# Performance work log

Hardware: AMD Instinct MI355X
Metric: run time of the kernel (lower is better)

The kernel has to match this reference:

```python
import jax, jax.numpy as jnp
import numpy as np

EPS = 1e-5

def layer_norm(x, g, b):
    m = x.mean(-1, keepdims=True)
    v = ((x - m) ** 2).mean(-1, keepdims=True)
    return (x - m) * jax.lax.rsqrt(v + EPS) * g + b

def setup_inputs() -> dict:
    key = jax.random.key(0)
    ks = jax.random.split(key, 12)
    H = 2048; E = 2048; I = 2048; N = 32
    A = (H + E) // 2  # attention hidden = 2048
    s = lambda fan: 1.0 / np.sqrt(fan)
    inp = {
        "input":   jax.random.normal(ks[0], (I,), jnp.float32),
        "hiddens": jax.random.normal(ks[1], (N, H), jnp.float32),
        "cells":   jax.random.normal(ks[2], (N, H), jnp.float32),
        "external":jax.random.normal(ks[3], (E,), jnp.float32),
        # weights (torch nn.Linear layout: [out, in]); LN enabled -> no biases on linears
        "W_ai":   jax.random.uniform(ks[4], (A, H + E), jnp.float32, -s(H+E), s(H+E)),
        "W_attn": jax.random.uniform(ks[5], (1, A), jnp.float32, -s(A), s(A)),
        "W_merge":jax.random.uniform(ks[6], (H, H), jnp.float32, -s(H), s(H)),
        "W_iou":  jax.random.uniform(ks[7], (3 * H, I + H), jnp.float32, -s(I+H), s(I+H)),
        "W_fi":   jax.random.uniform(ks[8], (H, I), jnp.float32, -s(I), s(I)),
        "W_fh":   jax.random.uniform(ks[9], (H, H), jnp.float32, -s(H), s(H)),
        "g_merge": jnp.ones((H,), jnp.float32), "b_merge": jnp.zeros((H,), jnp.float32),
        "g_f": jnp.ones((H,), jnp.float32), "b_f": jnp.zeros((H,), jnp.float32),
        "g_i": jnp.ones((H,), jnp.float32), "b_i": jnp.zeros((H,), jnp.float32),
        "g_o": jnp.ones((H,), jnp.float32), "b_o": jnp.zeros((H,), jnp.float32),
        "g_u": jnp.ones((H,), jnp.float32), "b_u": jnp.zeros((H,), jnp.float32),
        "g_c": jnp.ones((H,), jnp.float32), "b_c": jnp.zeros((H,), jnp.float32),
    }
    return inp

def reference(input, hiddens, cells, external,
              W_ai, W_attn, W_merge, W_iou, W_fi, W_fh,
              g_merge, b_merge, g_f, b_f, g_i, b_i, g_o, b_o, g_u, b_u, g_c, b_c):
    N, H = hiddens.shape
    # forget-gate preactivations: [H] + [N,H] -> [N,H]
    f_lin = input @ W_fi.T + hiddens @ W_fh.T
    # attentive merge over children
    ext = jnp.broadcast_to(external, (N, external.shape[0]))
    ai = jnp.tanh(jnp.concatenate([hiddens, ext], axis=1) @ W_ai.T)       # [N, (H+E)//2]
    attn = jax.nn.softmax(ai @ W_attn.T, axis=0)                          # [N, 1]
    merged = (hiddens * attn).sum(0)                                      # [H]
    merge_hidden = jnp.tanh(layer_norm(merged @ W_merge.T, g_merge, b_merge))
    # i/o/u gates from [input ; merged_hidden]
    iou = jnp.concatenate([input, merge_hidden]) @ W_iou.T                # [3H]
    i_l, o_l, u_l = jnp.split(iou, 3)
    f = jax.nn.sigmoid(layer_norm(f_lin, g_f, b_f))                       # [N,H]
    i = jax.nn.sigmoid(layer_norm(i_l, g_i, b_i))
    o = jax.nn.sigmoid(layer_norm(o_l, g_o, b_o))
    u = jnp.tanh(layer_norm(u_l, g_u, b_u))                               # dropout=0 -> identity
    new_cell = layer_norm(i * u + (f * cells).sum(0), g_c, b_c)           # [H]
    new_h = o * jnp.tanh(new_cell)
    return new_h, new_cell
```

## Files before the change

kernel.cpp:

```cpp
#include <hip/hip_runtime.h>
#include <hip/hip_bf16.h>

typedef __bf16 bf16_t;
typedef __attribute__((ext_vector_type(8))) __bf16 bf16x8;
typedef __attribute__((ext_vector_type(4))) float f32x4;

#define EPSF 1e-5f

__global__ __launch_bounds__(256) void s1_mega(
    const float* __restrict__ hiddens, const float* __restrict__ external,
    const float* __restrict__ input,
    const float* __restrict__ W_ai, const float* __restrict__ W_fh,
    const float* __restrict__ W_fi, const float* __restrict__ W_attn,
    float* __restrict__ lp, float* __restrict__ fh_out, float* __restrict__ fi_out)
{
    __shared__ float red[4][16][16];
    __shared__ float ejs[4][16];

    int b    = blockIdx.x;
    int tid  = threadIdx.x;
    int wave = tid >> 6;
    int lane = tid & 63;

    if (b < 512) {
        bool is_ai = (b < 256);
        int  bb    = is_ai ? b : b - 256;
        int  jt    = bb & 127;
        int  nt    = bb >> 7;
        int  l15   = lane & 15;
        int  quad  = lane >> 4;
        int  k0    = wave * 512;
        int  wstride = is_ai ? 4096 : 2048;
        const float* W = is_ai ? W_ai : W_fh;

        const float* ap = hiddens + (size_t)(nt * 16 + l15) * 2048 + quad * 8 + k0;
        const float* bp = W + (size_t)(jt * 16 + l15) * wstride + quad * 8 + k0;

        f32x4 acc = {0.f, 0.f, 0.f, 0.f};
        float ejacc = 0.f;

        if (is_ai) {
            const float* ep = bp + 2048;
            const float* xp = external + quad * 8 + k0;
            #pragma unroll 2
            for (int k = 0; k < 512; k += 32) {
                float4 a0 = *(const float4*)(ap + k);
                float4 a1 = *(const float4*)(ap + k + 4);
                float4 b0 = *(const float4*)(bp + k);
                float4 b1 = *(const float4*)(bp + k + 4);
                bf16x8 av, bv;
                av[0]=(bf16_t)a0.x; av[1]=(bf16_t)a0.y; av[2]=(bf16_t)a0.z; av[3]=(bf16_t)a0.w;
                av[4]=(bf16_t)a1.x; av[5]=(bf16_t)a1.y; av[6]=(bf16_t)a1.z; av[7]=(bf16_t)a1.w;
                bv[0]=(bf16_t)b0.x; bv[1]=(bf16_t)b0.y; bv[2]=(bf16_t)b0.z; bv[3]=(bf16_t)b0.w;
                bv[4]=(bf16_t)b1.x; bv[5]=(bf16_t)b1.y; bv[6]=(bf16_t)b1.z; bv[7]=(bf16_t)b1.w;
                acc = __builtin_amdgcn_mfma_f32_16x16x32_bf16(av, bv, acc, 0, 0, 0);
                float4 e0 = *(const float4*)(ep + k);
                float4 e1 = *(const float4*)(ep + k + 4);
                float4 x0 = *(const float4*)(xp + k);
                float4 x1 = *(const float4*)(xp + k + 4);
                ejacc += e0.x*x0.x + e0.y*x0.y + e0.z*x0.z + e0.w*x0.w
                       + e1.x*x1.x + e1.y*x1.y + e1.z*x1.z + e1.w*x1.w;
            }
            ejacc += __shfl_xor(ejacc, 16, 64);
            ejacc += __shfl_xor(ejacc, 32, 64);
            if (quad == 0) ejs[wave][l15] = ejacc;
        } else {
            #pragma unroll 4
            for (int k = 0; k < 512; k += 32) {
                float4 a0 = *(const float4*)(ap + k);
                float4 a1 = *(const float4*)(ap + k + 4);
                float4 b0 = *(const float4*)(bp + k);
                float4 b1 = *(const float4*)(bp + k + 4);
                bf16x8 av, bv;
                av[0]=(bf16_t)a0.x; av[1]=(bf16_t)a0.y; av[2]=(bf16_t)a0.z; av[3]=(bf16_t)a0.w;
                av[4]=(bf16_t)a1.x; av[5]=(bf16_t)a1.y; av[6]=(bf16_t)a1.z; av[7]=(bf16_t)a1.w;
                bv[0]=(bf16_t)b0.x; bv[1]=(bf16_t)b0.y; bv[2]=(bf16_t)b0.z; bv[3]=(bf16_t)b0.w;
                bv[4]=(bf16_t)b1.x; bv[5]=(bf16_t)b1.y; bv[6]=(bf16_t)b1.z; bv[7]=(bf16_t)b1.w;
                acc = __builtin_amdgcn_mfma_f32_16x16x32_bf16(av, bv, acc, 0, 0, 0);
            }
        }

        #pragma unroll
        for (int r = 0; r < 4; ++r) red[wave][quad * 4 + r][l15] = acc[r];
        __syncthreads();

        int row = tid >> 4, col = tid & 15;
        float s = red[0][row][col] + red[1][row][col] + red[2][row][col] + red[3][row][col];

        if (is_ai) {
            float ej = ejs[0][col] + ejs[1][col] + ejs[2][col] + ejs[3][col];
            float lg = tanhf(s + ej) * W_attn[jt * 16 + col];
            lg += __shfl_xor(lg, 1, 64);
            lg += __shfl_xor(lg, 2, 64);
            lg += __shfl_xor(lg, 4, 64);
            lg += __shfl_xor(lg, 8, 64);
            if (col == 0) lp[jt * 32 + nt * 16 + row] = lg;
        } else {
            fh_out[(size_t)(nt * 16 + row) * 2048 + jt * 16 + col] = s;
        }
    } else {
        int b2 = b - 512;
        #pragma unroll
        for (int r = 0; r < 4; ++r) {
            int row = b2 * 16 + wave * 4 + r;
            const float4* wp = (const float4*)(W_fi + (size_t)row * 2048) + lane;
            const float4* xp = (const float4*)input + lane;
            float acc2 = 0.f;
            #pragma unroll
            for (int k = 0; k < 512; k += 64) {
                float4 w = wp[k];
                float4 v = xp[k];
                acc2 += w.x*v.x + w.y*v.y + w.z*v.z + w.w*v.w;
            }
            #pragma unroll
            for (int off = 32; off; off >>= 1) acc2 += __shfl_down(acc2, off, 64);
            if (lane == 0) fi_out[row] = acc2;
        }
    }
}

__global__ __launch_bounds__(256) void s2_mega(
    const float* __restrict__ fi, const float* __restrict__ fh,
    const float* __restrict__ lp, const float* __restrict__ hiddens,
    float* __restrict__ frs, float* __restrict__ merged)
{
    __shared__ float s1[256], s2[256];
    int b = blockIdx.x, t = threadIdx.x;

    if (b < 32) {
        int n = b;
        float sum = 0.f, sq = 0.f;
        #pragma unroll
        for (int i = 0; i < 8; ++i) {
            int h = t * 8 + i;
            float v = fi[h] + fh[n * 2048 + h];
            sum += v; sq += v * v;
        }
        s1[t] = sum; s2[t] = sq;
        __syncthreads();
        for (int off = 128; off; off >>= 1) {
            if (t < off) { s1[t] += s1[t + off]; s2[t] += s2[t + off]; }
            __syncthreads();
        }
        if (t == 0) {
            const float inv = 1.f / 2048.f;
            float mean = s1[0] * inv;
            frs[n * 2]     = mean;
            frs[n * 2 + 1] = rsqrtf(s2[0] * inv - mean * mean + EPSF);
        }
    } else {
        __shared__ float lred[32][8];
        __shared__ float attnw[32];
        int n = t >> 3, sl = t & 7;
        float p = 0.f;
        #pragma unroll
        for (int m = 0; m < 16; ++m) p += lp[(sl * 16 + m) * 32 + n];
        lred[n][sl] = p;
        __syncthreads();
        if (sl == 0) {
            float lg = 0.f;
            #pragma unroll
            for (int m = 0; m < 8; ++m) lg += lred[n][m];
            lred[n][0] = lg;
        }
        __syncthreads();
        if (t < 32) {
            float mx = -1e30f;
            for (int m = 0; m < 32; ++m) mx = fmaxf(mx, lred[m][0]);
            float ssum = 0.f;
            for (int m = 0; m < 32; ++m) ssum += expf(lred[m][0] - mx);
            attnw[t] = expf(lred[t][0] - mx) / ssum;
        }
        __syncthreads();
        int h = (b - 32) * 256 + t;
        float acc = 0.f;
        #pragma unroll 8
        for (int n2 = 0; n2 < 32; ++n2) acc += attnw[n2] * hiddens[n2 * 2048 + h];
        merged[h] = acc;
    }
}

__global__ __launch_bounds__(256) void s3_mega(
    const float* __restrict__ W_merge, const float* __restrict__ merged,
    const float* __restrict__ fi, const float* __restrict__ fh,
    const float* __restrict__ frs, const float* __restrict__ gf,
    const float* __restrict__ bf_, const float* __restrict__ cells,
    float* __restrict__ mm, float* __restrict__ fc)
{
    int b = blockIdx.x, t = threadIdx.x;
    if (b < 512) {
        int row  = b * 4 + (t >> 6);
        int lane = t & 63;
        const float4* wp = (const float4*)(W_merge + (size_t)row * 2048) + lane;
        const float4* xp = (const float4*)merged + lane;
        float acc = 0.f;
        #pragma unroll
        for (int k = 0; k < 512; k += 64) {
            float4 w = wp[k];
            float4 v = xp[k];
            acc += w.x*v.x + w.y*v.y + w.z*v.z + w.w*v.w;
        }
        #pragma unroll
        for (int off = 32; off; off >>= 1) acc += __shfl_down(acc, off, 64);
        if (lane == 0) mm[row] = acc;
    } else {
        int h = (b - 512) * 256 + t;
        float g = gf[h], bb = bf_[h], f_i = fi[h];
        float acc = 0.f;
        for (int n = 0; n < 32; ++n) {
            float v = (f_i + fh[n * 2048 + h] - frs[n * 2]) * frs[n * 2 + 1] * g + bb;
            float f = 1.f / (1.f + expf(-v));
            acc += f * cells[n * 2048 + h];
        }
        fc[h] = acc;
    }
}

__global__ __launch_bounds__(256) void s4_iou(
    const float* __restrict__ W_iou, const float* __restrict__ mm,
    const float* __restrict__ input, const float* __restrict__ g,
    const float* __restrict__ bvec, float* __restrict__ iou)
{
    __shared__ float xcat[4096];
    __shared__ float s1[256], s2[256];
    int b = blockIdx.x, t = threadIdx.x;

    float v[8]; float sum = 0.f, sq = 0.f;
    #pragma unroll
    for (int i = 0; i < 8; ++i) {
        v[i] = mm[t * 8 + i]; sum += v[i]; sq += v[i] * v[i];
    }
    s1[t] = sum; s2[t] = sq;
    __syncthreads();
    for (int off = 128; off; off >>= 1) {
        if (t < off) { s1[t] += s1[t + off]; s2[t] += s2[t + off]; }
        __syncthreads();
    }
    const float inv = 1.f / 2048.f;
    float mean = s1[0] * inv;
    float r = rsqrtf(s2[0] * inv - mean * mean + EPSF);
    #pragma unroll
    for (int i = 0; i < 8; ++i) {
        int h = t * 8 + i;
        xcat[h]        = input[h];
        xcat[2048 + h] = tanhf((v[i] - mean) * r * g[h] + bvec[h]);
    }
    __syncthreads();

    int wave = t >> 6, lane = t & 63;
    int row = b * 4 + wave;
    const float4* wp = (const float4*)(W_iou + (size_t)row * 4096) + lane;
    const float4* xp = (const float4*)xcat + lane;
    float acc = 0.f;
    #pragma unroll
    for (int k = 0; k < 1024; k += 64) {
        float4 w = wp[k];
        float4 x = xp[k];
        acc += w.x*x.x + w.y*x.y + w.z*x.z + w.w*x.w;
    }
    #pragma unroll
    for (int off = 32; off; off >>= 1) acc += __shfl_down(acc, off, 64);
    if (lane == 0) iou[row] = acc;
}

__global__ __launch_bounds__(256) void s5_tail(
    const float* __restrict__ iou, const float* __restrict__ fc,
    const float* __restrict__ gi, const float* __restrict__ bi,
    const float* __restrict__ go, const float* __restrict__ bo,
    const float* __restrict__ gu, const float* __restrict__ bu,
    const float* __restrict__ gc, const float* __restrict__ bc,
    float* __restrict__ out)
{
    __shared__ float sA[6][256];
    int t = threadIdx.x;
    float vi[8], vo[8], vu[8];
    float si = 0, qi = 0, so = 0, qo = 0, su = 0, qu = 0;
    #pragma unroll
    for (int i = 0; i < 8; ++i) {
        int h = t * 8 + i;
        vi[i] = iou[h]; vo[i] = iou[2048 + h]; vu[i] = iou[4096 + h];
        si += vi[i]; qi += vi[i] * vi[i];
        so += vo[i]; qo += vo[i] * vo[i];
        su += vu[i]; qu += vu[i] * vu[i];
    }
    sA[0][t] = si; sA[1][t] = qi; sA[2][t] = so;
    sA[3][t] = qo; sA[4][t] = su; sA[5][t] = qu;
    __syncthreads();
    for (int off = 128; off; off >>= 1) {
        if (t < off) {
            #pragma unroll
            for (int c = 0; c < 6; ++c) sA[c][t] += sA[c][t + off];
        }
        __syncthreads();
    }
    const float inv = 1.f / 2048.f;
    float mi = sA[0][0] * inv, ri = rsqrtf(sA[1][0] * inv - mi * mi + EPSF);
    float mo = sA[2][0] * inv, ro = rsqrtf(sA[3][0] * inv - mo * mo + EPSF);
    float mu = sA[4][0] * inv, ru = rsqrtf(sA[5][0] * inv - mu * mu + EPSF);
    __syncthreads();

    float o_[8], v_[8];
    float sv = 0, qv = 0;
    #pragma unroll
    for (int i = 0; i < 8; ++i) {
        int h = t * 8 + i;
        float ivl = 1.f / (1.f + expf(-((vi[i] - mi) * ri * gi[h] + bi[h])));
        o_[i]     = 1.f / (1.f + expf(-((vo[i] - mo) * ro * go[h] + bo[h])));
        float uvl = tanhf((vu[i] - mu) * ru * gu[h] + bu[h]);
        v_[i] = ivl * uvl + fc[h];
        sv += v_[i]; qv += v_[i] * v_[i];
    }
    sA[0][t] = sv; sA[1][t] = qv;
    __syncthreads();
    for (int off = 128; off; off >>= 1) {
        if (t < off) { sA[0][t] += sA[0][t + off]; sA[1][t] += sA[1][t + off]; }
        __syncthreads();
    }
    float mc = sA[0][0] * inv, rc = rsqrtf(sA[1][0] * inv - mc * mc + EPSF);
    #pragma unroll
    for (int i = 0; i < 8; ++i) {
        int h = t * 8 + i;
        float nc = (v_[i] - mc) * rc * gc[h] + bc[h];
        float nh = o_[i] * tanhf(nc);
        out[h]        = nh;
        out[2048 + h] = nc;
    }
}

extern "C" void kernel_launch(void* const* d_in, const int* in_sizes, int n_in,
                              void* d_out, int out_size, void* d_ws, size_t ws_size,
                              hipStream_t stream)
{
    const float* input    = (const float*)d_in[0];
    const float* hiddens  = (const float*)d_in[1];
    const float* cells    = (const float*)d_in[2];
    const float* external = (const float*)d_in[3];
    const float* W_ai     = (const float*)d_in[4];
    const float* W_attn   = (const float*)d_in[5];
    const float* W_merge  = (const float*)d_in[6];
    const float* W_iou    = (const float*)d_in[7];
    const float* W_fi     = (const float*)d_in[8];
    const float* W_fh     = (const float*)d_in[9];
    const float* g_merge  = (const float*)d_in[10];
    const float* b_merge  = (const float*)d_in[11];
    const float* g_f      = (const float*)d_in[12];
    const float* b_f      = (const float*)d_in[13];
    const float* g_i      = (const float*)d_in[14];
    const float* b_i      = (const float*)d_in[15];
    const float* g_o      = (const float*)d_in[16];
    const float* b_o      = (const float*)d_in[17];
    const float* g_u      = (const float*)d_in[18];
    const float* b_u      = (const float*)d_in[19];
    const float* g_c      = (const float*)d_in[20];
    const float* b_c      = (const float*)d_in[21];

    float* ws = (float*)d_ws;
    float* ws_fh     = ws;
    float* ws_fi     = ws + 65536;
    float* ws_lp     = ws + 67584;
    float* ws_frs    = ws + 71680;
    float* ws_merged = ws + 71744;
    float* ws_mm     = ws + 73792;
    float* ws_fc     = ws + 75840;
    float* ws_iou    = ws + 77888;
    float* out = (float*)d_out;

    s1_mega<<<640, 256, 0, stream>>>(hiddens, external, input,
                                     W_ai, W_fh, W_fi, W_attn,
                                     ws_lp, ws_fh, ws_fi);
    s2_mega<<<40, 256, 0, stream>>>(ws_fi, ws_fh, ws_lp, hiddens,
                                    ws_frs, ws_merged);
    s3_mega<<<520, 256, 0, stream>>>(W_merge, ws_merged, ws_fi, ws_fh,
                                     ws_frs, g_f, b_f, cells, ws_mm, ws_fc);
    s4_iou<<<1536, 256, 0, stream>>>(W_iou, ws_mm, input, g_merge, b_merge, ws_iou);
    s5_tail<<<1, 256, 0, stream>>>(ws_iou, ws_fc, g_i, b_i, g_o, b_o,
                                   g_u, b_u, g_c, b_c, out);
}
```

Before: 292.0 us.

## Process both child tiles per block in s1 and two rows per wave in s4

In s1, each MFMA block now computes both 16-row halves of the 32 children against one weight tile, so each W_ai/W_fh tile is loaded once instead of twice. The W_fi GEMV blocks are rebalanced to fill the freed grid slots. In s4, the LayerNorm reduction moves to per-wave shuffles with the activation vector kept in registers instead of shared memory, and each wave handles two rows, halving the grid. This trades higher register pressure and fewer blocks for fewer redundant weight reads and per-block setup passes.

```diff
diff --git a/kernel.cpp b/kernel.cpp
--- a/kernel.cpp
+++ b/kernel.cpp
@@ -14,7 +14,7 @@
     const float* __restrict__ W_fi, const float* __restrict__ W_attn,
     float* __restrict__ lp, float* __restrict__ fh_out, float* __restrict__ fi_out)
 {
-    __shared__ float red[4][16][16];
+    __shared__ float red[4][2][16][16];
     __shared__ float ejs[4][16];
 
     int b    = blockIdx.x;
@@ -22,21 +22,21 @@
     int wave = tid >> 6;
     int lane = tid & 63;
 
-    if (b < 512) {
-        bool is_ai = (b < 256);
-        int  bb    = is_ai ? b : b - 256;
-        int  jt    = bb & 127;
-        int  nt    = bb >> 7;
+    if (b < 256) {
+        bool is_ai = (b < 128);
+        int  jt    = is_ai ? b : b - 128;
         int  l15   = lane & 15;
         int  quad  = lane >> 4;
         int  k0    = wave * 512;
         int  wstride = is_ai ? 4096 : 2048;
         const float* W = is_ai ? W_ai : W_fh;
 
-        const float* ap = hiddens + (size_t)(nt * 16 + l15) * 2048 + quad * 8 + k0;
-        const float* bp = W + (size_t)(jt * 16 + l15) * wstride + quad * 8 + k0;
-
-        f32x4 acc = {0.f, 0.f, 0.f, 0.f};
+        const float* a0p = hiddens + (size_t)l15 * 2048 + quad * 8 + k0;
+        const float* a1p = hiddens + (size_t)(16 + l15) * 2048 + quad * 8 + k0;
+        const float* bp  = W + (size_t)(jt * 16 + l15) * wstride + quad * 8 + k0;
+
+        f32x4 acc0 = {0.f, 0.f, 0.f, 0.f};
+        f32x4 acc1 = {0.f, 0.f, 0.f, 0.f};
         float ejacc = 0.f;
 
         if (is_ai) {
@@ -44,20 +44,25 @@
             const float* xp = external + quad * 8 + k0;
             #pragma unroll 2
             for (int k = 0; k < 512; k += 32) {
-                float4 a0 = *(const float4*)(ap + k);
-                float4 a1 = *(const float4*)(ap + k + 4);
+                float4 p0 = *(const float4*)(a0p + k);
+                float4 p1 = *(const float4*)(a0p + k + 4);
+                float4 q0 = *(const float4*)(a1p + k);
+                float4 q1 = *(const float4*)(a1p + k + 4);
                 float4 b0 = *(const float4*)(bp + k);
                 float4 b1 = *(const float4*)(bp + k + 4);
-                bf16x8 av, bv;
-                av[0]=(bf16_t)a0.x; av[1]=(bf16_t)a0.y; av[2]=(bf16_t)a0.z; av[3]=(bf16_t)a0.w;
-                av[4]=(bf16_t)a1.x; av[5]=(bf16_t)a1.y; av[6]=(bf16_t)a1.z; av[7]=(bf16_t)a1.w;
-                bv[0]=(bf16_t)b0.x; bv[1]=(bf16_t)b0.y; bv[2]=(bf16_t)b0.z; bv[3]=(bf16_t)b0.w;
-                bv[4]=(bf16_t)b1.x; bv[5]=(bf16_t)b1.y; bv[6]=(bf16_t)b1.z; bv[7]=(bf16_t)b1.w;
-                acc = __builtin_amdgcn_mfma_f32_16x16x32_bf16(av, bv, acc, 0, 0, 0);
                 float4 e0 = *(const float4*)(ep + k);
                 float4 e1 = *(const float4*)(ep + k + 4);
                 float4 x0 = *(const float4*)(xp + k);
                 float4 x1 = *(const float4*)(xp + k + 4);
+                bf16x8 av0, av1, bv;
+                av0[0]=(bf16_t)p0.x; av0[1]=(bf16_t)p0.y; av0[2]=(bf16_t)p0.z; av0[3]=(bf16_t)p0.w;
+                av0[4]=(bf16_t)p1.x; av0[5]=(bf16_t)p1.y; av0[6]=(bf16_t)p1.z; av0[7]=(bf16_t)p1.w;
+                av1[0]=(bf16_t)q0.x; av1[1]=(bf16_t)q0.y; av1[2]=(bf16_t)q0.z; av1[3]=(bf16_t)q0.w;
+                av1[4]=(bf16_t)q1.x; av1[5]=(bf16_t)q1.y; av1[6]=(bf16_t)q1.z; av1[7]=(bf16_t)q1.w;
+                bv[0]=(bf16_t)b0.x; bv[1]=(bf16_t)b0.y; bv[2]=(bf16_t)b0.z; bv[3]=(bf16_t)b0.w;
+                bv[4]=(bf16_t)b1.x; bv[5]=(bf16_t)b1.y; bv[6]=(bf16_t)b1.z; bv[7]=(bf16_t)b1.w;
+                acc0 = __builtin_amdgcn_mfma_f32_16x16x32_bf16(av0, bv, acc0, 0, 0, 0);
+                acc1 = __builtin_amdgcn_mfma_f32_16x16x32_bf16(av1, bv, acc1, 0, 0, 0);
                 ejacc += e0.x*x0.x + e0.y*x0.y + e0.z*x0.z + e0.w*x0.w
                        + e1.x*x1.x + e1.y*x1.y + e1.z*x1.z + e1.w*x1.w;
             }
@@ -65,44 +70,57 @@
             ejacc += __shfl_xor(ejacc, 32, 64);
             if (quad == 0) ejs[wave][l15] = ejacc;
         } else {
-            #pragma unroll 4
+            #pragma unroll 2
             for (int k = 0; k < 512; k += 32) {
-                float4 a0 = *(const float4*)(ap + k);
-                float4 a1 = *(const float4*)(ap + k + 4);
+                float4 p0 = *(const float4*)(a0p + k);
+                float4 p1 = *(const float4*)(a0p + k + 4);
+                float4 q0 = *(const float4*)(a1p + k);
+                float4 q1 = *(const float4*)(a1p + k + 4);
                 float4 b0 = *(const float4*)(bp + k);
                 float4 b1 = *(const float4*)(bp + k + 4);
-                bf16x8 av, bv;
-                av[0]=(bf16_t)a0.x; av[1]=(bf16_t)a0.y; av[2]=(bf16_t)a0.z; av[3]=(bf16_t)a0.w;
-                av[4]=(bf16_t)a1.x; av[5]=(bf16_t)a1.y; av[6]=(bf16_t)a1.z; av[7]=(bf16_t)a1.w;
+                bf16x8 av0, av1, bv;
+                av0[0]=(bf16_t)p0.x; av0[1]=(bf16_t)p0.y; av0[2]=(bf16_t)p0.z; av0[3]=(bf16_t)p0.w;
+                av0[4]=(bf16_t)p1.x; av0[5]=(bf16_t)p1.y; av0[6]=(bf16_t)p1.z; av0[7]=(bf16_t)p1.w;
+                av1[0]=(bf16_t)q0.x; av1[1]=(bf16_t)q0.y; av1[2]=(bf16_t)q0.z; av1[3]=(bf16_t)q0.w;
+                av1[4]=(bf16_t)q1.x; av1[5]=(bf16_t)q1.y; av1[6]=(bf16_t)q1.z; av1[7]=(bf16_t)q1.w;
                 bv[0]=(bf16_t)b0.x; bv[1]=(bf16_t)b0.y; bv[2]=(bf16_t)b0.z; bv[3]=(bf16_t)b0.w;
                 bv[4]=(bf16_t)b1.x; bv[5]=(bf16_t)b1.y; bv[6]=(bf16_t)b1.z; bv[7]=(bf16_t)b1.w;
-                acc = __builtin_amdgcn_mfma_f32_16x16x32_bf16(av, bv, acc, 0, 0, 0);
+                acc0 = __builtin_amdgcn_mfma_f32_16x16x32_bf16(av0, bv, acc0, 0, 0, 0);
+                acc1 = __builtin_amdgcn_mfma_f32_16x16x32_bf16(av1, bv, acc1, 0, 0, 0);
             }
         }
 
         #pragma unroll
-        for (int r = 0; r < 4; ++r) red[wave][quad * 4 + r][l15] = acc[r];
+        for (int r = 0; r < 4; ++r) {
+            red[wave][0][quad * 4 + r][l15] = acc0[r];
+            red[wave][1][quad * 4 + r][l15] = acc1[r];
+        }
         __syncthreads();
 
         int row = tid >> 4, col = tid & 15;
-        float s = red[0][row][col] + red[1][row][col] + red[2][row][col] + red[3][row][col];
-
-        if (is_ai) {
-            float ej = ejs[0][col] + ejs[1][col] + ejs[2][col] + ejs[3][col];
-            float lg = tanhf(s + ej) * W_attn[jt * 16 + col];
-            lg += __shfl_xor(lg, 1, 64);
-            lg += __shfl_xor(lg, 2, 64);
-            lg += __shfl_xor(lg, 4, 64);
-            lg += __shfl_xor(lg, 8, 64);
-            if (col == 0) lp[jt * 32 + nt * 16 + row] = lg;
-        } else {
-            fh_out[(size_t)(nt * 16 + row) * 2048 + jt * 16 + col] = s;
+        #pragma unroll
+        for (int nt = 0; nt < 2; ++nt) {
+            float s = red[0][nt][row][col] + red[1][nt][row][col]
+                    + red[2][nt][row][col] + red[3][nt][row][col];
+            if (is_ai) {
+                float ej = ejs[0][col] + ejs[1][col] + ejs[2][col] + ejs[3][col];
+                float lg = tanhf(s + ej) * W_attn[jt * 16 + col];
+                lg += __shfl_xor(lg, 1, 64);
+                lg += __shfl_xor(lg, 2, 64);
+                lg += __shfl_xor(lg, 4, 64);
+                lg += __shfl_xor(lg, 8, 64);
+                if (col == 0) lp[jt * 32 + nt * 16 + row] = lg;
+            } else {
+                fh_out[(size_t)(nt * 16 + row) * 2048 + jt * 16 + col] = s;
+            }
         }
     } else {
-        int b2 = b - 512;
-        #pragma unroll
-        for (int r = 0; r < 4; ++r) {
-            int row = b2 * 16 + wave * 4 + r;
+        int nb = b - 256;
+        int base, nr;
+        if (nb < 128) { base = nb * 4;              nr = 1; }
+        else          { base = 512 + (nb - 128) * 12; nr = 3; }
+        for (int r = 0; r < nr; ++r) {
+            int row = base + wave * nr + r;
             const float4* wp = (const float4*)(W_fi + (size_t)row * 2048) + lane;
             const float4* xp = (const float4*)input + lane;
             float acc2 = 0.f;
@@ -216,51 +234,63 @@
     }
 }
 
-__global__ __launch_bounds__(256) void s4_iou(
+__global__ __launch_bounds__(256, 3) void s4_iou(
     const float* __restrict__ W_iou, const float* __restrict__ mm,
     const float* __restrict__ input, const float* __restrict__ g,
     const float* __restrict__ bvec, float* __restrict__ iou)
 {
-    __shared__ float xcat[4096];
-    __shared__ float s1[256], s2[256];
     int b = blockIdx.x, t = threadIdx.x;
-
-    float v[8]; float sum = 0.f, sq = 0.f;
-    #pragma unroll
-    for (int i = 0; i < 8; ++i) {
-        v[i] = mm[t * 8 + i]; sum += v[i]; sq += v[i] * v[i];
-    }
-    s1[t] = sum; s2[t] = sq;
-    __syncthreads();
-    for (int off = 128; off; off >>= 1) {
-        if (t < off) { s1[t] += s1[t + off]; s2[t] += s2[t + off]; }
-        __syncthreads();
+    int wave = t >> 6, lane = t & 63;
+
+    const float4* mm4 = (const float4*)mm;
+    const float4* in4 = (const float4*)input;
+    const float4* g4  = (const float4*)g;
+    const float4* b4  = (const float4*)bvec;
+
+    float4 mv[8];
+    #pragma unroll
+    for (int k = 0; k < 8; ++k) mv[k] = mm4[lane + 64 * k];
+    float sum = 0.f, sq = 0.f;
+    #pragma unroll
+    for (int k = 0; k < 8; ++k) {
+        sum += mv[k].x + mv[k].y + mv[k].z + mv[k].w;
+        sq  += mv[k].x*mv[k].x + mv[k].y*mv[k].y + mv[k].z*mv[k].z + mv[k].w*mv[k].w;
+    }
+    #pragma unroll
+    for (int off = 1; off < 64; off <<= 1) {
+        sum += __shfl_xor(sum, off, 64);
+        sq  += __shfl_xor(sq,  off, 64);
     }
     const float inv = 1.f / 2048.f;
-    float mean = s1[0] * inv;
-    float r = rsqrtf(s2[0] * inv - mean * mean + EPSF);
-    #pragma unroll
-    for (int i = 0; i < 8; ++i) {
-        int h = t * 8 + i;
-        xcat[h]        = input[h];
-        xcat[2048 + h] = tanhf((v[i] - mean) * r * g[h] + bvec[h]);
-    }
-    __syncthreads();
-
-    int wave = t >> 6, lane = t & 63;
-    int row = b * 4 + wave;
-    const float4* wp = (const float4*)(W_iou + (size_t)row * 4096) + lane;
-    const float4* xp = (const float4*)xcat + lane;
-    float acc = 0.f;
-    #pragma unroll
-    for (int k = 0; k < 1024; k += 64) {
-        float4 w = wp[k];
-        float4 x = xp[k];
-        acc += w.x*x.x + w.y*x.y + w.z*x.z + w.w*x.w;
-    }
-    #pragma unroll
-    for (int off = 32; off; off >>= 1) acc += __shfl_down(acc, off, 64);
-    if (lane == 0) iou[row] = acc;
+    float mean = sum * inv;
+    float r = rsqrtf(sq * inv - mean * mean + EPSF);
+
+    float4 xr[16];
+    #pragma unroll
+    for (int k = 0; k < 8; ++k) xr[k] = in4[lane + 64 * k];
+    #pragma unroll
+    for (int k = 0; k < 8; ++k) {
+        float4 gv = g4[lane + 64 * k];
+        float4 bv = b4[lane + 64 * k];
+        xr[8 + k].x = tanhf((mv[k].x - mean) * r * gv.x + bv.x);
+        xr[8 + k].y = tanhf((mv[k].y - mean) * r * gv.y + bv.y);
+        xr[8 + k].z = tanhf((mv[k].z - mean) * r * gv.z + bv.z);
+        xr[8 + k].w = tanhf((mv[k].w - mean) * r * gv.w + bv.w);
+    }
+
+    int row0 = (b * 4 + wave) * 2;
+    for (int rr = 0; rr < 2; ++rr) {
+        const float4* wp = (const float4*)(W_iou + (size_t)(row0 + rr) * 4096);
+        float acc = 0.f;
+        #pragma unroll
+        for (int k = 0; k < 16; ++k) {
+            float4 w = wp[lane + 64 * k];
+            acc += w.x*xr[k].x + w.y*xr[k].y + w.z*xr[k].z + w.w*xr[k].w;
+        }
+        #pragma unroll
+        for (int off = 32; off; off >>= 1) acc += __shfl_down(acc, off, 64);
+        if (lane == 0) iou[row0 + rr] = acc;
+    }
 }
 
 __global__ __launch_bounds__(256) void s5_tail(
@@ -365,14 +395,14 @@
     float* ws_iou    = ws + 77888;
     float* out = (float*)d_out;
 
-    s1_mega<<<640, 256, 0, stream>>>(hiddens, external, input,
+    s1_mega<<<512, 256, 0, stream>>>(hiddens, external, input,
                                      W_ai, W_fh, W_fi, W_attn,
                                      ws_lp, ws_fh, ws_fi);
     s2_mega<<<40, 256, 0, stream>>>(ws_fi, ws_fh, ws_lp, hiddens,
                                     ws_frs, ws_merged);
     s3_mega<<<520, 256, 0, stream>>>(W_merge, ws_merged, ws_fi, ws_fh,
                                      ws_frs, g_f, b_f, cells, ws_mm, ws_fc);
-    s4_iou<<<1536, 256, 0, stream>>>(W_iou, ws_mm, input, g_merge, b_merge, ws_iou);
+    s4_iou<<<768, 256, 0, stream>>>(W_iou, ws_mm, input, g_merge, b_merge, ws_iou);
     s5_tail<<<1, 256, 0, stream>>>(ws_iou, ws_fc, g_i, b_i, g_o, b_o,
                                    g_u, b_u, g_c, b_c, out);
 }
```

New measurement: 281.4 us. 3.6% less time.
